# Performance work log

Hardware: AMD Instinct MI355X
Metric: run time of the kernel (lower is better)

## Reference

```python
import jax, jax.numpy as jnp
import numpy as np

EPS = 1e-5

def _bn(h, gamma, beta):
    # BatchNorm1d in training mode: per-channel stats over the batch dim (L=1)
    m = jnp.mean(h, axis=0)
    v = jnp.var(h, axis=0)  # biased variance, as torch uses for normalization
    return gamma * (h - m) * jax.lax.rsqrt(v + EPS) + beta

def setup_inputs() -> dict:
    key = jax.random.key(0)
    ks = jax.random.split(key, 8)
    vocab, emb = 8192, 512
    inter = (vocab + emb) // 2  # 4352
    N = 8192
    x_t = jax.random.randint(ks[0], (N,), 0, vocab, dtype=jnp.int64)
    W1 = jax.random.normal(ks[1], (inter, vocab), dtype=jnp.float32) * 0.02
    b1 = jax.random.normal(ks[2], (inter,), dtype=jnp.float32) * 0.02
    g1 = jnp.ones((inter,), dtype=jnp.float32)
    beta1 = jnp.zeros((inter,), dtype=jnp.float32)
    W2 = jax.random.normal(ks[3], (emb, inter), dtype=jnp.float32) * 0.02
    b2 = jax.random.normal(ks[4], (emb,), dtype=jnp.float32) * 0.02
    g2 = jnp.ones((emb,), dtype=jnp.float32)
    beta2 = jnp.zeros((emb,), dtype=jnp.float32)
    return {"x_t": x_t, "W1": W1, "b1": b1, "g1": g1, "beta1": beta1,
            "W2": W2, "b2": b2, "g2": g2, "beta2": beta2}

def reference(x_t, W1, b1, g1, beta1, W2, b2, g2, beta2):
    # one_hot(x_t) @ Conv1d(k=1) weight == gather of W1 columns (same math, no dense one-hot)
    h1 = W1.T[x_t] + b1                      # [N, inter]
    h1 = jax.nn.gelu(_bn(h1, g1, beta1), approximate=False)
    h2 = h1 @ W2.T + b2                      # [N, emb]
    out = jax.nn.gelu(_bn(h2, g2, beta2), approximate=False)
    return out
```

## Files before the change

kernel.cpp:

```cpp
#include <hip/hip_runtime.h>
#include <hip/hip_bf16.h>
#include <math.h>

typedef __attribute__((ext_vector_type(8))) short short8;
typedef __attribute__((ext_vector_type(4))) float f32x4;

#define VOCAB 8192
#define NSAMP 8192
#define INTER 4352
#define EMB   512

#define OFF_CNT    0
#define OFF_A1     32768
#define OFF_M1     50176
#define OFF_S1     67584
#define OFF_S2     84992
#define OFF_A2     102400
#define OFF_M2     104448
#define OFF_PS1B   106496
#define OFF_PS2B   1155072
#define OFF_W2B    2203648
#define OFF_HACT   6660096
#define OFF_HPART  77963264
#define PART_BYTES 16777216ULL

__device__ __forceinline__ float gelu_exact(float x) {
    return 0.5f * x * (1.0f + erff(x * 0.70710678118654752f));
}
__device__ __forceinline__ unsigned short f2bf(float x) {
    __hip_bfloat16 b = __float2bfloat16(x);
    return *reinterpret_cast<unsigned short*>(&b);
}
__device__ __forceinline__ void async16(const unsigned short* g, unsigned short* l) {
    __builtin_amdgcn_global_load_lds(
        (const __attribute__((address_space(1))) void*)g,
        (__attribute__((address_space(3))) void*)l, 16, 0, 0);
}

__global__ void k_zero_cnt(int* cnt) {
    cnt[blockIdx.x * 256 + threadIdx.x] = 0;
}
__global__ void k_hist(const int* __restrict__ xt, int* __restrict__ cnt) {
    int n = blockIdx.x * 256 + threadIdx.x;
    atomicAdd(&cnt[xt[n]], 1);
}

__global__ __launch_bounds__(256) void k_stats1(const float* __restrict__ W1,
                                                const int* __restrict__ cnt,
                                                float* __restrict__ s1o,
                                                float* __restrict__ s2o) {
    const int t = threadIdx.x, lane = t & 63, w = t >> 6;
    const int row = blockIdx.x * 4 + w;
    const float* wr = W1 + (size_t)row * VOCAB;
    float s1 = 0.f, s2 = 0.f;
    #pragma unroll 8
    for (int it = 0; it < 32; ++it) {
        int v = it * 256 + lane * 4;
        float4 x = *(const float4*)(wr + v);
        int4 c = *(const int4*)(cnt + v);
        float cx = (float)c.x, cy = (float)c.y, cz = (float)c.z, cw = (float)c.w;
        s1 += cx * x.x + cy * x.y + cz * x.z + cw * x.w;
        s2 += cx * x.x * x.x + cy * x.y * x.y + cz * x.z * x.z + cw * x.w * x.w;
    }
    #pragma unroll
    for (int d = 1; d < 64; d <<= 1) {
        s1 += __shfl_xor(s1, d);
        s2 += __shfl_xor(s2, d);
    }
    if (lane == 0) { s1o[row] = s1; s2o[row] = s2; }
}

__global__ void k_stats1f(const float* __restrict__ s1, const float* __restrict__ s2,
                          const float* __restrict__ g1, float* __restrict__ a1,
                          float* __restrict__ m1) {
    int i = blockIdx.x * 256 + threadIdx.x;
    float m = s1[i] * (1.f / NSAMP);
    float var = s2[i] * (1.f / NSAMP) - m * m;
    a1[i] = g1[i] * rsqrtf(var + 1e-5f);
    m1[i] = m;
}

__global__ __launch_bounds__(256) void k_build(const float* __restrict__ W1,
                                               const float* __restrict__ a1,
                                               const float* __restrict__ m1,
                                               const float* __restrict__ beta1,
                                               unsigned short* __restrict__ Hact) {
    const int i0 = blockIdx.x * 64;
    const int v0 = blockIdx.y * 256;
    const int t = threadIdx.x;
    const int c0 = (t & 15) * 4;
    const int vg = (t >> 4) * 4;
    float4 av = *(const float4*)(a1 + i0 + c0);
    float4 mv = *(const float4*)(m1 + i0 + c0);
    float4 bv = *(const float4*)(beta1 + i0 + c0);
    const float* ap = (const float*)&av;
    const float* mp = (const float*)&mv;
    const float* bp = (const float*)&bv;
    #pragma unroll
    for (int vi = 0; vi < 4; ++vi) {
        int vb = v0 + vi * 64 + vg;
        float wf[4][4];
        #pragma unroll
        for (int j = 0; j < 4; ++j)
            *(float4*)&wf[j][0] = *(const float4*)(W1 + (size_t)(i0 + c0 + j) * VOCAB + vb);
        #pragma unroll
        for (int k = 0; k < 4; ++k) {
            ushort4 o;
            o.x = f2bf(gelu_exact(ap[0] * (wf[0][k] - mp[0]) + bp[0]));
            o.y = f2bf(gelu_exact(ap[1] * (wf[1][k] - mp[1]) + bp[1]));
            o.z = f2bf(gelu_exact(ap[2] * (wf[2][k] - mp[2]) + bp[2]));
            o.w = f2bf(gelu_exact(ap[3] * (wf[3][k] - mp[3]) + bp[3]));
            *(ushort4*)&Hact[(size_t)(vb + k) * INTER + i0 + c0] = o;
        }
    }
}

__global__ void k_w2bf(const float* __restrict__ W2, unsigned short* __restrict__ W2b) {
    int idx = (blockIdx.x * 256 + threadIdx.x) * 4;
    float4 w = *(const float4*)(W2 + idx);
    ushort4 u;
    u.x = f2bf(w.x); u.y = f2bf(w.y); u.z = f2bf(w.z); u.w = f2bf(w.w);
    *(ushort4*)(W2b + idx) = u;
}

__global__ __launch_bounds__(256) void k_gemm(const unsigned short* __restrict__ A,
                                              const unsigned short* __restrict__ B,
                                              float* __restrict__ Cp, int kPer) {
    __shared__ __align__(16) unsigned short sA[128 * 64];
    __shared__ __align__(16) unsigned short sB[128 * 64];
    const int m0 = blockIdx.x * 128;
    const int n0 = blockIdx.y * 128;
    const int kbeg = blockIdx.z * kPer;
    const int kend = kbeg + kPer;
    float* C = Cp + (size_t)blockIdx.z * NSAMP * EMB;
    const int t = threadIdx.x;
    const int lane = t & 63;
    const int wave = t >> 6;
    const int wr = wave >> 1, wc = wave & 1;
    const int mq = lane & 15, kq = lane >> 4;
    const int srow = lane >> 3;
    const int scol = (lane & 7) * 8;
    f32x4 acc[4][4];
    #pragma unroll
    for (int r = 0; r < 4; ++r)
        #pragma unroll
        for (int c = 0; c < 4; ++c) acc[r][c] = (f32x4){0.f, 0.f, 0.f, 0.f};
    for (int k0 = kbeg; k0 < kend; k0 += 64) {
        #pragma unroll
        for (int p = 0; p < 4; ++p) {
            int r0 = (p * 4 + wave) * 8;
            async16(A + (size_t)(m0 + r0 + srow) * INTER + k0 + scol, &sA[r0 * 64]);
            async16(B + (size_t)(n0 + r0 + srow) * INTER + k0 + scol, &sB[r0 * 64]);
        }
        __syncthreads();
        #pragma unroll
        for (int kk = 0; kk < 64; kk += 32) {
            short8 af[4], bf[4];
            #pragma unroll
            for (int r = 0; r < 4; ++r)
                af[r] = *(const short8*)&sA[(wr * 64 + r * 16 + mq) * 64 + kk + kq * 8];
            #pragma unroll
            for (int c = 0; c < 4; ++c)
                bf[c] = *(const short8*)&sB[(wc * 64 + c * 16 + mq) * 64 + kk + kq * 8];
            #pragma unroll
            for (int r = 0; r < 4; ++r)
                #pragma unroll
                for (int c = 0; c < 4; ++c)
                    acc[r][c] = __builtin_amdgcn_mfma_f32_16x16x32_bf16(af[r], bf[c], acc[r][c], 0, 0, 0);
        }
        __syncthreads();
    }
    #pragma unroll
    for (int r = 0; r < 4; ++r) {
        #pragma unroll
        for (int c = 0; c < 4; ++c) {
            int col = n0 + wc * 64 + c * 16 + mq;
            int rowb = m0 + wr * 64 + r * 16 + kq * 4;
            #pragma unroll
            for (int j = 0; j < 4; ++j)
                C[(size_t)(rowb + j) * EMB + col] = acc[r][c][j];
        }
    }
}

__global__ __launch_bounds__(256) void k_reduce(const float* hpart,
                                                const int* __restrict__ cnt,
                                                float* h2,
                                                float* __restrict__ ps1,
                                                float* __restrict__ ps2, int S) {
    __shared__ float4 b1[128], b2[128];
    const int v0 = blockIdx.x * 16;
    const int t = threadIdx.x;
    const int half = t >> 7;
    const int c4 = (t & 127) * 4;
    float4 acc1 = {0.f, 0.f, 0.f, 0.f}, acc2 = {0.f, 0.f, 0.f, 0.f};
    #pragma unroll
    for (int rp = 0; rp < 8; ++rp) {
        int v = v0 + rp * 2 + half;
        size_t off = (size_t)v * EMB + c4;
        float4 h = *(const float4*)(hpart + off);
        for (int s = 1; s < S; ++s) {
            float4 hs = *(const float4*)(hpart + (size_t)s * NSAMP * EMB + off);
            h.x += hs.x; h.y += hs.y; h.z += hs.z; h.w += hs.w;
        }
        *(float4*)(h2 + off) = h;
        float w = (float)cnt[v];
        acc1.x += w * h.x; acc1.y += w * h.y; acc1.z += w * h.z; acc1.w += w * h.w;
        acc2.x += w * h.x * h.x; acc2.y += w * h.y * h.y;
        acc2.z += w * h.z * h.z; acc2.w += w * h.w * h.w;
    }
    if (half == 1) { b1[t & 127] = acc1; b2[t & 127] = acc2; }
    __syncthreads();
    if (half == 0) {
        float4 o1 = b1[t & 127], o2 = b2[t & 127];
        o1.x += acc1.x; o1.y += acc1.y; o1.z += acc1.z; o1.w += acc1.w;
        o2.x += acc2.x; o2.y += acc2.y; o2.z += acc2.z; o2.w += acc2.w;
        ps1[(size_t)(c4 + 0) * 512 + blockIdx.x] = o1.x;
        ps1[(size_t)(c4 + 1) * 512 + blockIdx.x] = o1.y;
        ps1[(size_t)(c4 + 2) * 512 + blockIdx.x] = o1.z;
        ps1[(size_t)(c4 + 3) * 512 + blockIdx.x] = o1.w;
        ps2[(size_t)(c4 + 0) * 512 + blockIdx.x] = o2.x;
        ps2[(size_t)(c4 + 1) * 512 + blockIdx.x] = o2.y;
        ps2[(size_t)(c4 + 2) * 512 + blockIdx.x] = o2.z;
        ps2[(size_t)(c4 + 3) * 512 + blockIdx.x] = o2.w;
    }
}

__global__ __launch_bounds__(256) void k_stats2f(const float* __restrict__ ps1,
                                                 const float* __restrict__ ps2,
                                                 const float* __restrict__ g2,
                                                 float* __restrict__ a2,
                                                 float* __restrict__ m2) {
    const int lane = threadIdx.x & 63;
    const int e = blockIdx.x * 4 + (threadIdx.x >> 6);
    float s1 = 0.f, s2 = 0.f;
    #pragma unroll
    for (int k = 0; k < 8; ++k) {
        s1 += ps1[(size_t)e * 512 + k * 64 + lane];
        s2 += ps2[(size_t)e * 512 + k * 64 + lane];
    }
    #pragma unroll
    for (int d = 1; d < 64; d <<= 1) {
        s1 += __shfl_xor(s1, d);
        s2 += __shfl_xor(s2, d);
    }
    if (lane == 0) {
        float m = s1 * (1.f / NSAMP);
        float var = s2 * (1.f / NSAMP) - m * m;
        a2[e] = g2[e] * rsqrtf(var + 1e-5f);
        m2[e] = m;
    }
}

__global__ __launch_bounds__(256) void k_final(const float* __restrict__ h2,
                                               const int* __restrict__ xt,
                                               const float* __restrict__ a2,
                                               const float* __restrict__ m2,
                                               const float* __restrict__ beta2,
                                               float* __restrict__ out) {
    const int t = threadIdx.x;
    const int n = blockIdx.x * 2 + (t >> 7);
    const int e = (t & 127) * 4;
    const int v = xt[n];
    float4 h = *(const float4*)(h2 + (size_t)v * EMB + e);
    float4 a = *(const float4*)(a2 + e);
    float4 m = *(const float4*)(m2 + e);
    float4 b = *(const float4*)(beta2 + e);
    float4 o;
    o.x = gelu_exact(a.x * (h.x - m.x) + b.x);
    o.y = gelu_exact(a.y * (h.y - m.y) + b.y);
    o.z = gelu_exact(a.z * (h.z - m.z) + b.z);
    o.w = gelu_exact(a.w * (h.w - m.w) + b.w);
    *(float4*)(out + (size_t)n * EMB + e) = o;
}

extern "C" void kernel_launch(void* const* d_in, const int* in_sizes, int n_in,
                              void* d_out, int out_size, void* d_ws, size_t ws_size,
                              hipStream_t stream) {
    const int* xt      = (const int*)d_in[0];
    const float* W1    = (const float*)d_in[1];
    const float* g1    = (const float*)d_in[3];
    const float* beta1 = (const float*)d_in[4];
    const float* W2    = (const float*)d_in[5];
    const float* g2    = (const float*)d_in[7];
    const float* beta2 = (const float*)d_in[8];
    float* out = (float*)d_out;

    char* ws = (char*)d_ws;
    int*   cnt  = (int*)  (ws + OFF_CNT);
    float* a1   = (float*)(ws + OFF_A1);
    float* m1   = (float*)(ws + OFF_M1);
    float* s1   = (float*)(ws + OFF_S1);
    float* s2   = (float*)(ws + OFF_S2);
    float* a2   = (float*)(ws + OFF_A2);
    float* m2   = (float*)(ws + OFF_M2);
    float* ps1b = (float*)(ws + OFF_PS1B);
    float* ps2b = (float*)(ws + OFF_PS2B);
    unsigned short* W2b  = (unsigned short*)(ws + OFF_W2B);
    unsigned short* Hact = (unsigned short*)(ws + OFF_HACT);
    float* hpart = (float*)(ws + OFF_HPART);
    float* h2 = hpart;

    int S = 1;
    if (ws_size >= OFF_HPART + 4 * PART_BYTES) S = 4;
    else if (ws_size >= OFF_HPART + 2 * PART_BYTES) S = 2;

    k_zero_cnt<<<32, 256, 0, stream>>>(cnt);
    k_hist<<<32, 256, 0, stream>>>(xt, cnt);
    k_stats1<<<1088, 256, 0, stream>>>(W1, cnt, s1, s2);
    k_stats1f<<<17, 256, 0, stream>>>(s1, s2, g1, a1, m1);
    k_build<<<dim3(68, 32), 256, 0, stream>>>(W1, a1, m1, beta1, Hact);
    k_w2bf<<<2176, 256, 0, stream>>>(W2, W2b);
    k_gemm<<<dim3(64, 4, S), 256, 0, stream>>>(Hact, W2b, hpart, INTER / S);
    k_reduce<<<512, 256, 0, stream>>>(hpart, cnt, h2, ps1b, ps2b, S);
    k_stats2f<<<128, 256, 0, stream>>>(ps1b, ps2b, g2, a2, m2);
    k_final<<<4096, 256, 0, stream>>>(h2, xt, a2, m2, beta2, out);
}
```

Baseline: 369.5 us.

## Widen GEMM tile to full EMB, swizzle LDS, fuse stats finalize, skip zero-count rows

The GEMM now computes a 128x512 output tile per 512-thread block, so each A tile is loaded once rather than four times. LDS reads and writes use an XOR swizzle to avoid bank conflicts. The BN1 finalize step is folded into k_stats1, which removes one launch. The reduce kernel skips vocab rows with zero count. The trade-off is more accumulator registers and LDS per block, lower occupancy, and only 64*S blocks in the GEMM grid, which may underfill the GPU's compute units.

```diff
diff --git a/kernel.cpp b/kernel.cpp
--- a/kernel.cpp
+++ b/kernel.cpp
@@ -13,15 +13,13 @@
 #define OFF_CNT    0
 #define OFF_A1     32768
 #define OFF_M1     50176
-#define OFF_S1     67584
-#define OFF_S2     84992
-#define OFF_A2     102400
-#define OFF_M2     104448
-#define OFF_PS1B   106496
-#define OFF_PS2B   1155072
-#define OFF_W2B    2203648
-#define OFF_HACT   6660096
-#define OFF_HPART  77963264
+#define OFF_A2     67584
+#define OFF_M2     69632
+#define OFF_PS1B   71680
+#define OFF_PS2B   1120256
+#define OFF_W2B    2168832
+#define OFF_HACT   6625280
+#define OFF_HPART  77928448
 #define PART_BYTES 16777216ULL
 
 __device__ __forceinline__ float gelu_exact(float x) {
@@ -47,8 +45,9 @@
 
 __global__ __launch_bounds__(256) void k_stats1(const float* __restrict__ W1,
                                                 const int* __restrict__ cnt,
-                                                float* __restrict__ s1o,
-                                                float* __restrict__ s2o) {
+                                                const float* __restrict__ g1,
+                                                float* __restrict__ a1,
+                                                float* __restrict__ m1) {
     const int t = threadIdx.x, lane = t & 63, w = t >> 6;
     const int row = blockIdx.x * 4 + w;
     const float* wr = W1 + (size_t)row * VOCAB;
@@ -67,17 +66,12 @@
         s1 += __shfl_xor(s1, d);
         s2 += __shfl_xor(s2, d);
     }
-    if (lane == 0) { s1o[row] = s1; s2o[row] = s2; }
-}
-
-__global__ void k_stats1f(const float* __restrict__ s1, const float* __restrict__ s2,
-                          const float* __restrict__ g1, float* __restrict__ a1,
-                          float* __restrict__ m1) {
-    int i = blockIdx.x * 256 + threadIdx.x;
-    float m = s1[i] * (1.f / NSAMP);
-    float var = s2[i] * (1.f / NSAMP) - m * m;
-    a1[i] = g1[i] * rsqrtf(var + 1e-5f);
-    m1[i] = m;
+    if (lane == 0) {
+        float m = s1 * (1.f / NSAMP);
+        float var = s2 * (1.f / NSAMP) - m * m;
+        a1[row] = g1[row] * rsqrtf(var + 1e-5f);
+        m1[row] = m;
+    }
 }
 
 __global__ __launch_bounds__(256) void k_build(const float* __restrict__ W1,
@@ -123,49 +117,55 @@
     *(ushort4*)(W2b + idx) = u;
 }
 
-__global__ __launch_bounds__(256) void k_gemm(const unsigned short* __restrict__ A,
+__global__ __launch_bounds__(512) void k_gemm(const unsigned short* __restrict__ A,
                                               const unsigned short* __restrict__ B,
                                               float* __restrict__ Cp, int kPer) {
     __shared__ __align__(16) unsigned short sA[128 * 64];
-    __shared__ __align__(16) unsigned short sB[128 * 64];
+    __shared__ __align__(16) unsigned short sB[512 * 64];
     const int m0 = blockIdx.x * 128;
-    const int n0 = blockIdx.y * 128;
     const int kbeg = blockIdx.z * kPer;
     const int kend = kbeg + kPer;
     float* C = Cp + (size_t)blockIdx.z * NSAMP * EMB;
     const int t = threadIdx.x;
     const int lane = t & 63;
     const int wave = t >> 6;
-    const int wr = wave >> 1, wc = wave & 1;
+    const int wr = wave >> 2, wc = wave & 3;
     const int mq = lane & 15, kq = lane >> 4;
     const int srow = lane >> 3;
-    const int scol = (lane & 7) * 8;
-    f32x4 acc[4][4];
+    const int sgrp = lane & 7;
+    const int scol = (sgrp ^ srow) * 8;
+    const int swz = mq & 7;
+    f32x4 acc[4][8];
     #pragma unroll
     for (int r = 0; r < 4; ++r)
         #pragma unroll
-        for (int c = 0; c < 4; ++c) acc[r][c] = (f32x4){0.f, 0.f, 0.f, 0.f};
+        for (int c = 0; c < 8; ++c) acc[r][c] = (f32x4){0.f, 0.f, 0.f, 0.f};
     for (int k0 = kbeg; k0 < kend; k0 += 64) {
         #pragma unroll
-        for (int p = 0; p < 4; ++p) {
-            int r0 = (p * 4 + wave) * 8;
+        for (int p = 0; p < 2; ++p) {
+            int r0 = wave * 16 + p * 8;
             async16(A + (size_t)(m0 + r0 + srow) * INTER + k0 + scol, &sA[r0 * 64]);
-            async16(B + (size_t)(n0 + r0 + srow) * INTER + k0 + scol, &sB[r0 * 64]);
+        }
+        #pragma unroll
+        for (int p = 0; p < 8; ++p) {
+            int r0 = wave * 64 + p * 8;
+            async16(B + (size_t)(r0 + srow) * INTER + k0 + scol, &sB[r0 * 64]);
         }
         __syncthreads();
         #pragma unroll
         for (int kk = 0; kk < 64; kk += 32) {
-            short8 af[4], bf[4];
+            const int gbase = kq + (kk >> 3);
+            short8 af[4], bf[8];
             #pragma unroll
             for (int r = 0; r < 4; ++r)
-                af[r] = *(const short8*)&sA[(wr * 64 + r * 16 + mq) * 64 + kk + kq * 8];
+                af[r] = *(const short8*)&sA[(wr * 64 + r * 16 + mq) * 64 + ((gbase ^ swz) * 8)];
             #pragma unroll
-            for (int c = 0; c < 4; ++c)
-                bf[c] = *(const short8*)&sB[(wc * 64 + c * 16 + mq) * 64 + kk + kq * 8];
+            for (int c = 0; c < 8; ++c)
+                bf[c] = *(const short8*)&sB[(wc * 128 + c * 16 + mq) * 64 + ((gbase ^ swz) * 8)];
             #pragma unroll
             for (int r = 0; r < 4; ++r)
                 #pragma unroll
-                for (int c = 0; c < 4; ++c)
+                for (int c = 0; c < 8; ++c)
                     acc[r][c] = __builtin_amdgcn_mfma_f32_16x16x32_bf16(af[r], bf[c], acc[r][c], 0, 0, 0);
         }
         __syncthreads();
@@ -173,8 +173,8 @@
     #pragma unroll
     for (int r = 0; r < 4; ++r) {
         #pragma unroll
-        for (int c = 0; c < 4; ++c) {
-            int col = n0 + wc * 64 + c * 16 + mq;
+        for (int c = 0; c < 8; ++c) {
+            int col = wc * 128 + c * 16 + mq;
             int rowb = m0 + wr * 64 + r * 16 + kq * 4;
             #pragma unroll
             for (int j = 0; j < 4; ++j)
@@ -196,18 +196,21 @@
     float4 acc1 = {0.f, 0.f, 0.f, 0.f}, acc2 = {0.f, 0.f, 0.f, 0.f};
     #pragma unroll
     for (int rp = 0; rp < 8; ++rp) {
-        int v = v0 + rp * 2 + half;
-        size_t off = (size_t)v * EMB + c4;
-        float4 h = *(const float4*)(hpart + off);
-        for (int s = 1; s < S; ++s) {
-            float4 hs = *(const float4*)(hpart + (size_t)s * NSAMP * EMB + off);
-            h.x += hs.x; h.y += hs.y; h.z += hs.z; h.w += hs.w;
-        }
-        *(float4*)(h2 + off) = h;
-        float w = (float)cnt[v];
-        acc1.x += w * h.x; acc1.y += w * h.y; acc1.z += w * h.z; acc1.w += w * h.w;
-        acc2.x += w * h.x * h.x; acc2.y += w * h.y * h.y;
-        acc2.z += w * h.z * h.z; acc2.w += w * h.w * h.w;
+        int r = v0 + rp * 2 + half;
+        int cw_i = cnt[r];
+        if (cw_i > 0) {
+            size_t off = (size_t)r * EMB + c4;
+            float4 h = *(const float4*)(hpart + off);
+            for (int s = 1; s < S; ++s) {
+                float4 hs = *(const float4*)(hpart + (size_t)s * NSAMP * EMB + off);
+                h.x += hs.x; h.y += hs.y; h.z += hs.z; h.w += hs.w;
+            }
+            *(float4*)(h2 + off) = h;
+            float w = (float)cw_i;
+            acc1.x += w * h.x; acc1.y += w * h.y; acc1.z += w * h.z; acc1.w += w * h.w;
+            acc2.x += w * h.x * h.x; acc2.y += w * h.y * h.y;
+            acc2.z += w * h.z * h.z; acc2.w += w * h.w * h.w;
+        }
     }
     if (half == 1) { b1[t & 127] = acc1; b2[t & 127] = acc2; }
     __syncthreads();
@@ -290,8 +293,6 @@
     int*   cnt  = (int*)  (ws + OFF_CNT);
     float* a1   = (float*)(ws + OFF_A1);
     float* m1   = (float*)(ws + OFF_M1);
-    float* s1   = (float*)(ws + OFF_S1);
-    float* s2   = (float*)(ws + OFF_S2);
     float* a2   = (float*)(ws + OFF_A2);
     float* m2   = (float*)(ws + OFF_M2);
     float* ps1b = (float*)(ws + OFF_PS1B);
@@ -307,11 +308,10 @@
 
     k_zero_cnt<<<32, 256, 0, stream>>>(cnt);
     k_hist<<<32, 256, 0, stream>>>(xt, cnt);
-    k_stats1<<<1088, 256, 0, stream>>>(W1, cnt, s1, s2);
-    k_stats1f<<<17, 256, 0, stream>>>(s1, s2, g1, a1, m1);
+    k_stats1<<<1088, 256, 0, stream>>>(W1, cnt, g1, a1, m1);
     k_build<<<dim3(68, 32), 256, 0, stream>>>(W1, a1, m1, beta1, Hact);
     k_w2bf<<<2176, 256, 0, stream>>>(W2, W2b);
-    k_gemm<<<dim3(64, 4, S), 256, 0, stream>>>(Hact, W2b, hpart, INTER / S);
+    k_gemm<<<dim3(64, 1, S), 512, 0, stream>>>(Hact, W2b, hpart, INTER / S);
     k_reduce<<<512, 256, 0, stream>>>(hpart, cnt, h2, ps1b, ps2b, S);
     k_stats2f<<<128, 256, 0, stream>>>(ps1b, ps2b, g2, a2, m2);
     k_final<<<4096, 256, 0, stream>>>(h2, xt, a2, m2, beta2, out);
```

New measurement: 356.3 us. -3.6%, faster.
